# Kernel optimization log

Hardware: AMD Instinct MI355X
Metric: run time of the kernel (lower is better)

Reference implementation:

```python
import jax, jax.numpy as jnp
import numpy as np

B, S1, S2, H, DW = 64, 512, 512, 768, 200


def setup_inputs() -> dict:
    key = jax.random.key(0)
    ks = jax.random.split(key, 16)
    inp = {
        'x1': jax.random.normal(ks[0], (B, S1, H), jnp.float32),
        'x1_h': jax.random.normal(ks[1], (B, H), jnp.float32),
        'x1_mask': jax.random.randint(ks[2], (B, S1), 0, 2, jnp.int32),
        'y': jax.random.normal(ks[3], (B, S1), jnp.float32),
        'x2': jax.random.normal(ks[4], (B, S2, H), jnp.float32),
        'x2_h': jax.random.normal(ks[5], (B, H), jnp.float32),
        'x2_mask': jax.random.randint(ks[6], (B, S2), 0, 2, jnp.int32),
        'tt': jax.random.normal(ks[7], (B, S1, DW), jnp.float32),
        'tt2': jax.random.normal(ks[8], (B, S2, DW), jnp.float32),
        # parameters (xavier ~ N(0, 2/(fan_in+fan_out)))
        'W_bert': jax.random.normal(ks[9], (H + 1, H), jnp.float32) * np.sqrt(2.0 / (H + 1 + H)),
        'W_wv': jax.random.normal(ks[10], (DW + 1, DW), jnp.float32) * np.sqrt(2.0 / (DW + 1 + DW)),
        'lin_wv_w': jax.random.normal(ks[11], (DW, H), jnp.float32) * np.sqrt(1.0 / DW),
        'lin_wv_b': jnp.zeros((H,), jnp.float32),
        'lin_w': jax.random.normal(ks[12], (4 * H, 1), jnp.float32) * np.sqrt(1.0 / (4 * H)),
        'lin_b': jnp.zeros((1,), jnp.float32),
    }
    return inp


def _branch(x_cat, W, keys_vals, x1_inv, x2_inv):
    # x_cat: [B,S1,D+1], W: [D+1,D], keys_vals: [B,S2,D]
    xw = jnp.matmul(x_cat, W)                                  # [B,S1,D]
    a = jnp.einsum('bsd,btd->bst', xw, keys_vals)              # [B,S1,S2]
    a = jnp.where(x2_inv[:, None, :], jnp.float32(-1e-5), a)   # faithful: tiny mask value, pre-softmax
    a = jax.nn.softmax(a, axis=-1)
    v = jnp.einsum('bst,btd->bsd', a, keys_vals)               # [B,S1,D]
    v = jnp.where(x1_inv[:, :, None], jnp.float32(-1e5), v)
    return v.max(axis=1)                                       # max-pool over S1 -> [B,D]


def reference(x1, x1_h, x1_mask, y, x2, x2_h, x2_mask, tt, tt2,
              W_bert, W_wv, lin_wv_w, lin_wv_b, lin_w, lin_b):
    x1_inv = (1 - x1_mask).astype(bool)  # True where padded
    x2_inv = (1 - x2_mask).astype(bool)

    # word-vector branch
    x1_wv = jnp.concatenate([tt, y[:, :, None]], axis=-1)      # [B,S1,201]
    x12_wv = _branch(x1_wv, W_wv, tt2, x1_inv, x2_inv)         # [B,200]
    x12_wv = x12_wv @ lin_wv_w + lin_wv_b                      # [B,768]

    # bert branch
    x1c = jnp.concatenate([x1, y[:, :, None]], axis=-1)        # [B,S1,769]
    x12 = _branch(x1c, W_bert, x2, x1_inv, x2_inv)             # [B,768]

    h = jnp.concatenate([x1_h, x2_h, x12, x12_wv], axis=1)     # [B,3072]
    o = jax.nn.sigmoid(h @ lin_w + lin_b)                      # [B,1]
    return (o, x1_inv.astype(jnp.int32), x2_inv.astype(jnp.int32))
```

## Files before the change

### kernel.cpp

```cpp
#include <hip/hip_runtime.h>


#define BB 64
#define SS 512
#define HH 768
#define DWW 200

typedef __attribute__((ext_vector_type(8))) _Float16 f16x8;
typedef __attribute__((ext_vector_type(4))) _Float16 f16x4;
typedef __attribute__((ext_vector_type(4))) float f32x4;
typedef unsigned int u32;

__device__ __forceinline__ u32 fkey(float f) {
    u32 u = __float_as_uint(f);
    return (u & 0x80000000u) ? ~u : (u | 0x80000000u);
}
__device__ __forceinline__ float fdec(u32 k) {
    u32 u = (k & 0x80000000u) ? (k & 0x7fffffffu) : ~k;
    return __uint_as_float(u);
}
__device__ __forceinline__ f32x4 mm(f16x8 a, f16x8 b, f32x4 c) {
    return __builtin_amdgcn_mfma_f32_16x16x32_f16(a, b, c, 0, 0, 0);
}
__device__ __forceinline__ void gl16(const void* g, void* l) {
    __builtin_amdgcn_global_load_lds(
        (const __attribute__((address_space(1))) void*)g,
        (__attribute__((address_space(3))) void*)l, 16, 0, 0);
}

__global__ __launch_bounds__(64) void k_setup(
    const int* __restrict__ m1, const int* __restrict__ m2,
    int* __restrict__ idx1, int* __restrict__ rcnt1,
    int* __restrict__ idx2, int* __restrict__ rcnt2) {
    int bid = blockIdx.x, lane = threadIdx.x;
    int b = bid & 63;
    const int* m = (bid < 64) ? m1 : m2;
    int* idx = (bid < 64) ? idx1 : idx2;
    int* rcnt = (bid < 64) ? rcnt1 : rcnt2;
    int base = 0;
#pragma unroll
    for (int c = 0; c < 8; ++c) {
        int s = c * 64 + lane;
        int v = m[b * SS + s];
        unsigned long long bal = __ballot(v != 0);
        int pre = __popcll(bal & ((1ull << lane) - 1ull));
        if (v) idx[b * SS + base + pre] = s;
        base += __popcll(bal);
    }
    if (lane == 0) rcnt[b] = base;
}

__global__ __launch_bounds__(256) void k_prep(
    const float* __restrict__ x2, const float* __restrict__ tt2,
    const float* __restrict__ x1, const float* __restrict__ tt,
    const float* __restrict__ yv,
    const int* __restrict__ m1, const int* __restrict__ m2,
    const float* __restrict__ Wb, const float* __restrict__ Wwv,
    const int* __restrict__ idx1, const int* __restrict__ rcnt1,
    const int* __restrict__ idx2, const int* __restrict__ rcnt2,
    _Float16* __restrict__ kvB, _Float16* __restrict__ kvTB,
    _Float16* __restrict__ kvW, _Float16* __restrict__ kvTW,
    _Float16* __restrict__ XcB, _Float16* __restrict__ XcW,
    float* __restrict__ out, u32* __restrict__ k1, u32* __restrict__ k2,
    _Float16* __restrict__ wbTH, _Float16* __restrict__ wwTH,
    int cb, int b0) {
    __shared__ float tile[64][65];
    int bx = blockIdx.x, tid = threadIdx.x;
    int NKV = cb * 128, NXC = cb * 256;

    if (bx < NKV) {
        int cbi = bx >> 7, sub = bx & 127;
        int t0 = (sub & 7) * 64, ybr = sub >> 3;
        const float* src; _Float16* kv; _Float16* kvT; int D, DPAD, DTPAD, d0;
        if (ybr < 12) { src = x2;  kv = kvB; kvT = kvTB; D = 768; DPAD = 768; DTPAD = 768; d0 = ybr * 64; }
        else          { src = tt2; kv = kvW; kvT = kvTW; D = 200; DPAD = 256; DTPAD = 256; d0 = (ybr - 12) * 64; }
        int bg = b0 + cbi;
        int rc2 = rcnt2[bg];
        int tpad2 = (rc2 + 127) & ~127;
        if (t0 >= tpad2) return;
        int tq = tid >> 3, c8 = (tid & 7) * 8;
#pragma unroll
        for (int i = 0; i < 2; ++i) {
            int t = tq + i * 32;
            int tg = t0 + t;
            int gd = d0 + c8;
            float v[8] = {0.f, 0.f, 0.f, 0.f, 0.f, 0.f, 0.f, 0.f};
            if (tg < rc2) {
                int sg = idx2[bg * SS + tg];
                const float* rp = src + ((size_t)bg * SS + sg) * D + gd;
                if (gd + 7 < D) {
                    float4 p0 = *(const float4*)(rp);
                    float4 p1 = *(const float4*)(rp + 4);
                    v[0] = p0.x; v[1] = p0.y; v[2] = p0.z; v[3] = p0.w;
                    v[4] = p1.x; v[5] = p1.y; v[6] = p1.z; v[7] = p1.w;
                } else {
#pragma unroll
                    for (int j = 0; j < 8; ++j) {
                        int d = gd + j;
                        v[j] = (d < D) ? src[((size_t)bg * SS + sg) * D + d] : 0.f;
                    }
                }
            }
            f16x8 o;
#pragma unroll
            for (int j = 0; j < 8; ++j) {
                tile[t][c8 + j] = v[j];
                o[j] = (_Float16)v[j];
            }
            *(f16x8*)(kv + ((size_t)cbi * SS + tg) * DPAD + gd) = o;
        }
        __syncthreads();
#pragma unroll
        for (int i = 0; i < 2; ++i) {
            int dl = tq + i * 32, gdr = d0 + dl;
            if (gdr < DTPAD) {
                f16x8 o;
#pragma unroll
                for (int j = 0; j < 8; ++j) o[j] = (_Float16)tile[c8 + j][dl];
                *(f16x8*)(kvT + ((size_t)cbi * DTPAD + gdr) * SS + t0 + c8) = o;
            }
        }
    } else if (bx < NKV + NXC) {
        int u = bx - NKV;
        int cbi = u >> 8, xb = u & 255;
        int bg = b0 + cbi;
        const float* X; _Float16* outp; int Din, KPAD; size_t ost;
        if (xb < 200) { X = x1; outp = XcB; Din = 768; KPAD = 800; ost = (size_t)cbi * 409600; }
        else { xb -= 200; X = tt; outp = XcW; Din = 200; KPAD = 224; ost = (size_t)cbi * 114688; }
        int i8 = (xb * 256 + tid) * 8;
        int s = i8 / KPAD, k0 = i8 - s * KPAD;
        int rc = rcnt1[bg];
        int rpad = (rc + 127) & ~127;
        if (s >= rpad) return;
        f16x8 o = {};
        if (s < rc) {
            int sg = idx1[bg * SS + s];
            const float* Xr = X + ((size_t)bg * SS + sg) * Din;
            if (k0 + 7 < Din) {
                float4 p0 = *(const float4*)(Xr + k0);
                float4 p1 = *(const float4*)(Xr + k0 + 4);
                o[0] = (_Float16)p0.x; o[1] = (_Float16)p0.y;
                o[2] = (_Float16)p0.z; o[3] = (_Float16)p0.w;
                o[4] = (_Float16)p1.x; o[5] = (_Float16)p1.y;
                o[6] = (_Float16)p1.z; o[7] = (_Float16)p1.w;
            } else {
#pragma unroll
                for (int j = 0; j < 8; ++j) {
                    int k = k0 + j;
                    float v = (k < Din) ? Xr[k]
                                        : ((k == Din) ? yv[(size_t)bg * SS + sg] : 0.f);
                    o[j] = (_Float16)v;
                }
            }
        }
        *(f16x8*)(outp + ost + (size_t)s * KPAD + k0) = o;
    } else {
        int u = bx - NKV - NXC;
        if (u < 128) {
            int i = u * 256 + tid;
            out[BB + i]           = (float)(1 - m1[i]);
            out[BB + BB * SS + i] = (float)(1 - m2[i]);
        } else if (u < 320) {
            int i = (u - 128) * 256 + tid;
            u32 v = fkey(-1e5f);
            if (i < BB * HH) k1[i] = v;
            if (i < BB * DWW) k2[i] = v;
        } else if (u < 920) {
            int i = ((u - 320) * 256 + tid) * 4;
            int n = i / 800, k = i - n * 800;
            f16x4 o;
#pragma unroll
            for (int j = 0; j < 4; ++j)
                o[j] = (_Float16)((k + j < 769) ? Wb[(size_t)(k + j) * 768 + n] : 0.f);
            *(f16x4*)(wbTH + i) = o;
        } else {
            int i = ((u - 920) * 256 + tid) * 4;
            int n = i / 224, k = i - n * 224;
            f16x4 o;
#pragma unroll
            for (int j = 0; j < 4; ++j)
                o[j] = (_Float16)((k + j < 201 && n < 200) ? Wwv[(size_t)(k + j) * 200 + n] : 0.f);
            *(f16x4*)(wwTH + i) = o;
        }
    }
}

template<int KA, int KST, int TN, int SXW, int DV, int AS, int BS, int EPI,
         bool GN, bool RK>
__device__ __forceinline__ void mm_core(
    const _Float16* __restrict__ A, const _Float16* __restrict__ B,
    _Float16* __restrict__ O, const float* __restrict__ rsum,
    u32* __restrict__ keys, int jb, const int* __restrict__ rcnt1,
    const int* __restrict__ rcnt2, int b0, char* lds, float* rsv) {
    int cbi = jb / (4 * TN);
    int rest = jb - cbi * (4 * TN);
    int ts = rest / TN, tn = rest - ts * TN;
    int s0 = ts * 128, n0 = tn * 128;

    int rc = rcnt1[b0 + cbi];
    int rpad = (rc + 127) & ~127;
    if (s0 >= rpad) return;
    if constexpr (GN) {
        int tp2 = (rcnt2[b0 + cbi] + 127) & ~127;
        if (n0 >= tp2) return;
    }

    int tid = threadIdx.x, lane = tid & 63, wid = tid >> 6;
    int wr = wid >> 1, wc = wid & 1;
    int l15 = lane & 15, sl = lane >> 4, gb = sl * 4;

    const _Float16* srcA = A + (size_t)cbi * AS + (size_t)s0 * KA;
    const _Float16* srcB = B + (size_t)cbi * BS + (size_t)n0 * KA;

    if constexpr (EPI == 2) {
        if (tid < 128) rsv[tid] = rsum[cbi * SS + s0 + tid];
    }

    f32x4 zz = {0.f, 0.f, 0.f, 0.f};
    f32x4 acc[4][4];
#pragma unroll
    for (int i = 0; i < 4; ++i)
#pragma unroll
        for (int j = 0; j < 4; ++j) acc[i][j] = zz;

#define STAGE(buf, ks)                                                        \
    _Pragma("unroll") for (int i = 0; i < 4; ++i) {                           \
        int c = wid + 4 * i;                                                  \
        int arr = c >> 3, sub = c & 7, slot = sub >> 1, rh = sub & 1;         \
        const _Float16* gp = (arr ? srcB : srcA) +                            \
            (size_t)(rh * 64 + lane) * KA + (ks) * 32 + slot * 8;             \
        gl16(gp, lds + (buf) * 16384 + c * 1024);                             \
    }
#define KBODY(ks, kend)                                                       \
    {                                                                         \
        if ((ks) + 1 < (kend)) STAGE(buf ^ 1, (ks) + 1);                      \
        char* base = lds + buf * 16384;                                       \
        f16x8 a[4], b[4];                                                     \
        _Pragma("unroll") for (int mf = 0; mf < 4; ++mf)                      \
            a[mf] = *(const f16x8*)(base + sl * 2048 +                        \
                                    (wr * 64 + mf * 16 + l15) * 16);          \
        _Pragma("unroll") for (int nf = 0; nf < 4; ++nf)                      \
            b[nf] = *(const f16x8*)(base + 8192 + sl * 2048 +                 \
                                    (wc * 64 + nf * 16 + l15) * 16);          \
        _Pragma("unroll") for (int mf = 0; mf < 4; ++mf)                      \
            _Pragma("unroll") for (int nf = 0; nf < 4; ++nf)                  \
                acc[mf][nf] = mm(a[mf], b[nf], acc[mf][nf]);                  \
        __syncthreads();                                                      \
        buf ^= 1;                                                             \
    }

    STAGE(0, 0);
    __syncthreads();
    int buf = 0;
    if constexpr (RK) {
        int kend = (rcnt2[b0 + cbi] + 31) >> 5;
        for (int ks = 0; ks < kend; ++ks) KBODY(ks, kend);
    } else {
#pragma unroll
        for (int ks = 0; ks < KST; ++ks) KBODY(ks, KST);
    }
#undef KBODY
#undef STAGE

    if constexpr (EPI == 1) {
        _Float16* ce = (_Float16*)lds;
#pragma unroll
        for (int mf = 0; mf < 4; ++mf)
#pragma unroll
            for (int nf = 0; nf < 4; ++nf)
#pragma unroll
                for (int r = 0; r < 4; ++r) {
                    int row = wr * 64 + mf * 16 + gb + r;
                    int col = wc * 64 + nf * 16 + l15;
                    ce[row * 128 + col] = (_Float16)acc[mf][nf][r];
                }
        __syncthreads();
#pragma unroll
        for (int i = 0; i < 8; ++i) {
            int t = tid + i * 256;
            int row = t >> 4, col = (t & 15) * 8;
            *(f16x8*)(O + ((size_t)cbi * SS + s0 + row) * SXW + n0 + col) =
                *(const f16x8*)(ce + row * 128 + col);
        }
    } else {
        int bg = b0 + cbi;
#pragma unroll
        for (int nf = 0; nf < 4; ++nf) {
            float mx = -3.0e38f;
#pragma unroll
            for (int mf = 0; mf < 4; ++mf)
#pragma unroll
                for (int r = 0; r < 4; ++r) {
                    int srow = wr * 64 + mf * 16 + gb + r;
                    if (s0 + srow < rc) mx = fmaxf(mx, acc[mf][nf][r] * rsv[srow]);
                }
            mx = fmaxf(mx, __shfl_xor(mx, 16));
            mx = fmaxf(mx, __shfl_xor(mx, 32));
            if (lane < 16) {
                int d = n0 + wc * 64 + nf * 16 + lane;
                if (d < DV) atomicMax(&keys[(size_t)bg * DV + d], fkey(mx));
            }
        }
    }
}

template<int EPI, bool GN, bool RK,
         int KA0, int KST0, int TN0, int SXW0, int DV0, int AS0, int BS0,
         int KA1, int KST1, int TN1, int SXW1, int DV1, int AS1, int BS1>
__global__ __launch_bounds__(256) void k_mmM(
    const _Float16* __restrict__ A0, const _Float16* __restrict__ B0,
    _Float16* __restrict__ O0, const float* __restrict__ rs0, u32* __restrict__ key0,
    const _Float16* __restrict__ A1, const _Float16* __restrict__ B1,
    _Float16* __restrict__ O1, const float* __restrict__ rs1, u32* __restrict__ key1,
    int nj0, const int* __restrict__ rcnt1, const int* __restrict__ rcnt2,
    int b0, int nwg) {
    __shared__ __align__(16) char lds[32768];
    __shared__ float rsv[128];
    int bid = blockIdx.x;
    int x = bid & 7, t = bid >> 3;
    int tb = nj0 >> 3;
    int tw = (nwg - nj0) >> 3;
    if (t < tb)
        mm_core<KA0, KST0, TN0, SXW0, DV0, AS0, BS0, EPI, GN, RK>(
            A0, B0, O0, rs0, key0, x * tb + t, rcnt1, rcnt2, b0, lds, rsv);
    else
        mm_core<KA1, KST1, TN1, SXW1, DV1, AS1, BS1, EPI, GN, RK>(
            A1, B1, O1, rs1, key1, x * tw + (t - tb), rcnt1, rcnt2, b0, lds, rsv);
}

__global__ __launch_bounds__(256) void k_softmaxM(
    _Float16* __restrict__ SP0, float* __restrict__ rs0,
    _Float16* __restrict__ SP1, float* __restrict__ rs1,
    const int* __restrict__ rcnt1, const int* __restrict__ rcnt2,
    int nblk0, int b0) {
    int bid = blockIdx.x;
    bool selw = bid >= nblk0;
    int b = selw ? bid - nblk0 : bid;
    _Float16* SP = selw ? SP1 : SP0;
    float* rs = selw ? rs1 : rs0;
    int cbi = b >> 7, rb = b & 127;
    int wid = threadIdx.x >> 6, lane = threadIdx.x & 63;
    int row = rb * 4 + wid, bg = b0 + cbi;
    int rc1 = rcnt1[bg];
    if (row >= rc1) return;
    int rc2 = rcnt2[bg];
    int col0 = lane * 8;
    f16x8 sv = *(const f16x8*)(SP + ((size_t)cbi * SS + row) * SS + col0);
    float mx = -3.0e38f;
    float c[8];
#pragma unroll
    for (int j = 0; j < 8; ++j) {
        c[j] = (float)sv[j];
        if (col0 + j < rc2) mx = fmaxf(mx, c[j]);
    }
#pragma unroll
    for (int off = 1; off <= 32; off <<= 1) mx = fmaxf(mx, __shfl_xor(mx, off));
    f16x8 o;
    float sm = 0.f;
#pragma unroll
    for (int j = 0; j < 8; ++j) {
        _Float16 h = (col0 + j < rc2) ? (_Float16)__expf(c[j] - mx) : (_Float16)0.f;
        o[j] = h;
        sm += (float)h;
    }
#pragma unroll
    for (int off = 1; off <= 32; off <<= 1) sm += __shfl_xor(sm, off);
    *(f16x8*)(SP + ((size_t)cbi * SS + row) * SS + col0) = o;
    if (lane == 0) rs[cbi * SS + row] = 1.0f / sm;
}

__global__ __launch_bounds__(256) void k_tail(
    const float* __restrict__ x1h, const float* __restrict__ x2h,
    const u32* __restrict__ keys, const u32* __restrict__ wvkeys,
    const float* __restrict__ Wp, const float* __restrict__ bp,
    const float* __restrict__ lw, const float* __restrict__ lb,
    float* __restrict__ out) {
    int b = blockIdx.x, tid = threadIdx.x;
    __shared__ float xv[DWW];
    __shared__ float wvp[HH];
    __shared__ float red[4];
    if (tid < DWW) xv[tid] = fdec(wvkeys[b * DWW + tid]);
    __syncthreads();
    for (int h = tid; h < HH; h += 256) {
        float acc = bp[h];
        for (int d = 0; d < DWW; ++d) acc += xv[d] * Wp[d * HH + h];
        wvp[h] = acc;
    }
    __syncthreads();
    float acc = 0.f;
    for (int i = tid; i < HH; i += 256) {
        acc += x1h[b * HH + i] * lw[i];
        acc += x2h[b * HH + i] * lw[HH + i];
        acc += fdec(keys[b * HH + i]) * lw[2 * HH + i];
        acc += wvp[i] * lw[3 * HH + i];
    }
    int wid = tid >> 6, lane = tid & 63;
#pragma unroll
    for (int off = 32; off; off >>= 1) acc += __shfl_down(acc, off);
    if (lane == 0) red[wid] = acc;
    __syncthreads();
    if (tid == 0) {
        float z = red[0] + red[1] + red[2] + red[3] + lb[0];
        out[b] = 1.f / (1.f + __expf(-z));
    }
}

extern "C" void kernel_launch(void* const* d_in, const int* in_sizes, int n_in,
                              void* d_out, int out_size, void* d_ws, size_t ws_size,
                              hipStream_t stream) {
    const float* x1   = (const float*)d_in[0];
    const float* x1h  = (const float*)d_in[1];
    const int*   m1   = (const int*)d_in[2];
    const float* y    = (const float*)d_in[3];
    const float* x2   = (const float*)d_in[4];
    const float* x2h  = (const float*)d_in[5];
    const int*   m2   = (const int*)d_in[6];
    const float* tt   = (const float*)d_in[7];
    const float* tt2  = (const float*)d_in[8];
    const float* Wb   = (const float*)d_in[9];
    const float* Wwv  = (const float*)d_in[10];
    const float* lwvw = (const float*)d_in[11];
    const float* lwvb = (const float*)d_in[12];
    const float* lw   = (const float*)d_in[13];
    const float* lb   = (const float*)d_in[14];
    float* out = (float*)d_out;
    char* ws = (char*)d_ws;

    u32*      x12key   = (u32*)ws;
    u32*      x12wvkey = (u32*)(ws + 196608);
    float*    rsumB    = (float*)(ws + 444416);
    float*    rsumW    = (float*)(ws + 575488);
    _Float16* wbTH     = (_Float16*)(ws + 706560);
    _Float16* wwTH     = (_Float16*)(ws + 1935360);
    int*      idx1Buf  = (int*)(ws + 2050048);
    int*      rcnt1Buf = (int*)(ws + 2181120);
    int*      idx2Buf  = (int*)(ws + 2181376);
    int*      rcnt2Buf = (int*)(ws + 2312448);
    const size_t D0 = 2312704;

    k_setup<<<128, 64, 0, stream>>>(m1, m2, idx1Buf, rcnt1Buf, idx2Buf, rcnt2Buf);

    const size_t perb = 4194304;
    int nb = 1;
    if (ws_size > D0 + perb) nb = (int)((ws_size - D0) / perb);
    if (nb > BB) nb = BB;
    if (nb < 1) nb = 1;

    char* R = ws + D0;
    _Float16* XcB = (_Float16*)R;
    _Float16* XcW = (_Float16*)(R + (size_t)nb * 819200);
    _Float16* S_b = (_Float16*)R;
    _Float16* S_w = (_Float16*)(R + (size_t)nb * 524288);
    char* p = R + (size_t)nb * 1048576;
    _Float16* XW_b = (_Float16*)p; p += (size_t)nb * 786432;
    _Float16* XW_w = (_Float16*)p; p += (size_t)nb * 262144;
    _Float16* KV_b = (_Float16*)p; p += (size_t)nb * 786432;
    _Float16* KV_w = (_Float16*)p; p += (size_t)nb * 262144;
    _Float16* KT_b = (_Float16*)p; p += (size_t)nb * 786432;
    _Float16* KT_w = (_Float16*)p;

    for (int b0 = 0; b0 < BB; b0 += nb) {
        int cb = (BB - b0 < nb) ? (BB - b0) : nb;
        int nprep = cb * 384 + ((b0 == 0) ? 976 : 0);
        k_prep<<<nprep, 256, 0, stream>>>(
            x2, tt2, x1, tt, y, m1, m2, Wb, Wwv,
            idx1Buf, rcnt1Buf, idx2Buf, rcnt2Buf,
            KV_b, KT_b, KV_w, KT_w, XcB, XcW,
            out, x12key, x12wvkey, wbTH, wwTH, cb, b0);
        k_mmM<1, false, false,
              800, 25, 6, 768, 0, 409600, 0,
              224,  7, 2, 256, 0, 114688, 0><<<cb * 32, 256, 0, stream>>>(
            XcB, wbTH, XW_b, nullptr, nullptr,
            XcW, wwTH, XW_w, nullptr, nullptr,
            cb * 24, rcnt1Buf, rcnt2Buf, b0, cb * 32);
        k_mmM<1, true, false,
              768, 24, 4, 512, 0, 393216, 393216,
              256,  8, 4, 512, 0, 131072, 131072><<<cb * 32, 256, 0, stream>>>(
            XW_b, KV_b, S_b, nullptr, nullptr,
            XW_w, KV_w, S_w, nullptr, nullptr,
            cb * 16, rcnt1Buf, rcnt2Buf, b0, cb * 32);
        k_softmaxM<<<cb * 256, 256, 0, stream>>>(
            S_b, rsumB, S_w, rsumW, rcnt1Buf, rcnt2Buf, cb * 128, b0);
        k_mmM<2, false, true,
              512, 16, 6, 0, 768, 262144, 393216,
              512, 16, 2, 0, 200, 262144, 131072><<<cb * 32, 256, 0, stream>>>(
            S_b, KT_b, nullptr, rsumB, x12key,
            S_w, KT_w, nullptr, rsumW, x12wvkey,
            cb * 24, rcnt1Buf, rcnt2Buf, b0, cb * 32);
    }

    k_tail<<<BB, 256, 0, stream>>>(x1h, x2h, x12key, x12wvkey,
                                   lwvw, lwvb, lw, lb, out);
}
```

Before: 270.0 us.

## Drop LDS double buffering in matmul core to halve shared memory

Replaces the double-buffered LDS staging in the MFMA matmul core with a single 16KB buffer. Each k-step now loads, syncs, computes and syncs again. The fp16 output epilogue writes in two 64-row halves so it fits in the smaller buffer. The goal is more resident workgroups per CU through lower LDS use, at the cost of losing overlap between global loads and MFMA compute and adding barriers.

```diff
diff --git a/kernel.cpp b/kernel.cpp
--- a/kernel.cpp
+++ b/kernel.cpp
@@ -223,41 +223,37 @@
 #pragma unroll
         for (int j = 0; j < 4; ++j) acc[i][j] = zz;
 
-#define STAGE(buf, ks)                                                        \
+#define STAGE(ks)                                                             \
     _Pragma("unroll") for (int i = 0; i < 4; ++i) {                           \
         int c = wid + 4 * i;                                                  \
         int arr = c >> 3, sub = c & 7, slot = sub >> 1, rh = sub & 1;         \
         const _Float16* gp = (arr ? srcB : srcA) +                            \
             (size_t)(rh * 64 + lane) * KA + (ks) * 32 + slot * 8;             \
-        gl16(gp, lds + (buf) * 16384 + c * 1024);                             \
-    }
-#define KBODY(ks, kend)                                                       \
+        gl16(gp, lds + c * 1024);                                             \
+    }
+#define KBODY(ks)                                                             \
     {                                                                         \
-        if ((ks) + 1 < (kend)) STAGE(buf ^ 1, (ks) + 1);                      \
-        char* base = lds + buf * 16384;                                       \
+        STAGE(ks);                                                            \
+        __syncthreads();                                                      \
         f16x8 a[4], b[4];                                                     \
         _Pragma("unroll") for (int mf = 0; mf < 4; ++mf)                      \
-            a[mf] = *(const f16x8*)(base + sl * 2048 +                        \
+            a[mf] = *(const f16x8*)(lds + sl * 2048 +                         \
                                     (wr * 64 + mf * 16 + l15) * 16);          \
         _Pragma("unroll") for (int nf = 0; nf < 4; ++nf)                      \
-            b[nf] = *(const f16x8*)(base + 8192 + sl * 2048 +                 \
+            b[nf] = *(const f16x8*)(lds + 8192 + sl * 2048 +                  \
                                     (wc * 64 + nf * 16 + l15) * 16);          \
         _Pragma("unroll") for (int mf = 0; mf < 4; ++mf)                      \
             _Pragma("unroll") for (int nf = 0; nf < 4; ++nf)                  \
                 acc[mf][nf] = mm(a[mf], b[nf], acc[mf][nf]);                  \
         __syncthreads();                                                      \
-        buf ^= 1;                                                             \
-    }
-
-    STAGE(0, 0);
-    __syncthreads();
-    int buf = 0;
+    }
+
     if constexpr (RK) {
         int kend = (rcnt2[b0 + cbi] + 31) >> 5;
-        for (int ks = 0; ks < kend; ++ks) KBODY(ks, kend);
+        for (int ks = 0; ks < kend; ++ks) KBODY(ks);
     } else {
 #pragma unroll
-        for (int ks = 0; ks < KST; ++ks) KBODY(ks, KST);
+        for (int ks = 0; ks < KST; ++ks) KBODY(ks);
     }
 #undef KBODY
 #undef STAGE
@@ -265,22 +261,28 @@
     if constexpr (EPI == 1) {
         _Float16* ce = (_Float16*)lds;
 #pragma unroll
-        for (int mf = 0; mf < 4; ++mf)
-#pragma unroll
-            for (int nf = 0; nf < 4; ++nf)
-#pragma unroll
-                for (int r = 0; r < 4; ++r) {
-                    int row = wr * 64 + mf * 16 + gb + r;
-                    int col = wc * 64 + nf * 16 + l15;
-                    ce[row * 128 + col] = (_Float16)acc[mf][nf][r];
-                }
-        __syncthreads();
-#pragma unroll
-        for (int i = 0; i < 8; ++i) {
-            int t = tid + i * 256;
-            int row = t >> 4, col = (t & 15) * 8;
-            *(f16x8*)(O + ((size_t)cbi * SS + s0 + row) * SXW + n0 + col) =
-                *(const f16x8*)(ce + row * 128 + col);
+        for (int half = 0; half < 2; ++half) {
+            if (wr == half) {
+#pragma unroll
+                for (int mf = 0; mf < 4; ++mf)
+#pragma unroll
+                    for (int nf = 0; nf < 4; ++nf)
+#pragma unroll
+                        for (int r = 0; r < 4; ++r) {
+                            int row = mf * 16 + gb + r;
+                            int col = wc * 64 + nf * 16 + l15;
+                            ce[row * 128 + col] = (_Float16)acc[mf][nf][r];
+                        }
+            }
+            __syncthreads();
+#pragma unroll
+            for (int i = 0; i < 4; ++i) {
+                int t = tid + i * 256;
+                int row = t >> 4, col = (t & 15) * 8;
+                *(f16x8*)(O + ((size_t)cbi * SS + s0 + half * 64 + row) * SXW +
+                          n0 + col) = *(const f16x8*)(ce + row * 128 + col);
+            }
+            __syncthreads();
         }
     } else {
         int bg = b0 + cbi;
@@ -314,7 +316,7 @@
     _Float16* __restrict__ O1, const float* __restrict__ rs1, u32* __restrict__ key1,
     int nj0, const int* __restrict__ rcnt1, const int* __restrict__ rcnt2,
     int b0, int nwg) {
-    __shared__ __align__(16) char lds[32768];
+    __shared__ __align__(16) char lds[16384];
     __shared__ float rsv[128];
     int bid = blockIdx.x;
     int x = bid & 7, t = bid >> 3;
```

Measured after the change: 268.5 us, median of 2. No clear change (-0.6%).
